# Kernel optimization log

Measured on AMD Instinct MI355X. Metric: run time of the kernel, lower is better.

The kernel has to match this reference:

```python
import jax, jax.numpy as jnp
import numpy as np

B, M = 16, 4096


def setup_inputs() -> dict:
    key = jax.random.key(0)
    k1, k2, k3, k4, k5 = jax.random.split(key, 5)
    return {
        "pred_R": jax.random.normal(k1, (B, 3, 3), dtype=jnp.float32),
        "pred_t": jax.random.normal(k2, (B, 3), dtype=jnp.float32),
        "gt_R": jax.random.normal(k3, (B, 3, 3), dtype=jnp.float32),
        "gt_t": jax.random.normal(k4, (B, 3), dtype=jnp.float32),
        "model_points": jax.random.normal(k5, (M, 3), dtype=jnp.float32),
    }


def reference(pred_R, pred_t, gt_R, gt_t, model_points):
    # Rigid transform: points @ R^T + t  -> [B, M, 3]
    pred = jnp.einsum('mk,bjk->bmj', model_points, pred_R) + pred_t[:, None, :]
    gt = jnp.einsum('mk,bjk->bmj', model_points, gt_R) + gt_t[:, None, :]
    # Pairwise squared L2 via ||a||^2 + ||b||^2 - 2 a.b (avoids [B,M,M,3] diff tensor)
    pn = jnp.sum(pred * pred, axis=-1)            # [B, M]
    gn = jnp.sum(gt * gt, axis=-1)                # [B, M]
    cross = jnp.einsum('bmk,bnk->bmn', pred, gt)  # [B, M, M]
    d2 = pn[:, :, None] + gn[:, None, :] - 2.0 * cross
    dist = jnp.sqrt(jnp.maximum(d2, 0.0))         # [B, M, M]
    min_dist = jnp.min(dist, axis=2)              # closest gt point per pred point
    return jnp.mean(min_dist)
```

## Files before the change

### kernel.cpp

```cpp
#include <hip/hip_runtime.h>
#include <hip/hip_bf16.h>
#include <float.h>

#define NB 16
#define MPTS 4096
#define NPRED (NB * MPTS)
#define GTQ 4
#define GTN 1024
#define NT 32
#define BLK 256
#define FRAGS 4
#define PREDS_PER_BLK 512
#define PGRP 8

typedef _Float16 half8 __attribute__((ext_vector_type(8)));
typedef float f32x16 __attribute__((ext_vector_type(16)));

__device__ inline void split16(float x, _Float16& hi, _Float16& lo) {
    hi = (_Float16)x;
    lo = (_Float16)(x - (float)hi);
}

__global__ __launch_bounds__(BLK) void adds_mfma(
    const float* __restrict__ pred_R, const float* __restrict__ pred_t,
    const float* __restrict__ gt_R,   const float* __restrict__ gt_t,
    const float* __restrict__ mp,     float* __restrict__ pmin,
    float* __restrict__ out)
{
    __shared__ half8 aT[NT * 64];

    const int bid = blockIdx.x;
    const int gtq = bid & (GTQ - 1);
    const int pg  = (bid >> 2) & (PGRP - 1);
    const int b   = bid >> 5;
    const int tid = threadIdx.x;
    const int ln  = tid & 63;
    const int wv  = tid >> 6;

    if (bid == 0 && tid == 0) out[0] = 0.0f;

    {
        float gR[9];
#pragma unroll
        for (int i = 0; i < 9; ++i) gR[i] = gt_R[b * 9 + i];
        const float gtx = gt_t[b * 3 + 0];
        const float gty = gt_t[b * 3 + 1];
        const float gtz = gt_t[b * 3 + 2];

#pragma unroll
        for (int w = 0; w < (NT * 64) / BLK; ++w) {
            const int v  = w * BLK + tid;
            const int t  = v >> 6;
            const int vl = v & 63;
            const int n  = gtq * GTN + t * 32 + (vl & 31);
            const float mx = mp[n * 3 + 0];
            const float my = mp[n * 3 + 1];
            const float mz = mp[n * 3 + 2];
            const float gx = fmaf(gR[0], mx, fmaf(gR[1], my, fmaf(gR[2], mz, gtx)));
            const float gy = fmaf(gR[3], mx, fmaf(gR[4], my, fmaf(gR[5], mz, gty)));
            const float gz = fmaf(gR[6], mx, fmaf(gR[7], my, fmaf(gR[8], mz, gtz)));
            const float gn = fmaf(gx, gx, fmaf(gy, gy, gz * gz));
            const float ux = -2.0f * gx, uy = -2.0f * gy, uz = -2.0f * gz;
            _Float16 hux, lux, huy, luy, huz, luz, gnh, gnl;
            split16(ux, hux, lux);
            split16(uy, huy, luy);
            split16(uz, huz, luz);
            split16(gn, gnh, gnl);
            half8 pk;
            if ((vl >> 5) == 0) {
                pk[0] = hux; pk[1] = huy; pk[2] = huz;
                pk[3] = hux; pk[4] = huy; pk[5] = huz;
                pk[6] = lux; pk[7] = luy;
            } else {
                pk[0] = luz; pk[1] = gnh; pk[2] = gnl;
                pk[3] = (_Float16)0.0f; pk[4] = (_Float16)0.0f;
                pk[5] = (_Float16)0.0f; pk[6] = (_Float16)0.0f;
                pk[7] = (_Float16)0.0f;
            }
            aT[v] = pk;
        }
    }

    float pR[9];
#pragma unroll
    for (int i = 0; i < 9; ++i) pR[i] = pred_R[b * 9 + i];
    const float ptx = pred_t[b * 3 + 0];
    const float pty = pred_t[b * 3 + 1];
    const float ptz = pred_t[b * 3 + 2];

    half8 bf[FRAGS];
    float pn[FRAGS];
    const int kh = ln >> 5;
#pragma unroll
    for (int f = 0; f < FRAGS; ++f) {
        const int predl = pg * PREDS_PER_BLK + wv * 128 + f * 32 + (ln & 31);
        const float mx = mp[predl * 3 + 0];
        const float my = mp[predl * 3 + 1];
        const float mz = mp[predl * 3 + 2];
        const float px = fmaf(pR[0], mx, fmaf(pR[1], my, fmaf(pR[2], mz, ptx)));
        const float py = fmaf(pR[3], mx, fmaf(pR[4], my, fmaf(pR[5], mz, pty)));
        const float pz = fmaf(pR[6], mx, fmaf(pR[7], my, fmaf(pR[8], mz, ptz)));
        pn[f] = fmaf(px, px, fmaf(py, py, pz * pz));
        _Float16 hpx, lpx, hpy, lpy, hpz, lpz;
        split16(px, hpx, lpx);
        split16(py, hpy, lpy);
        split16(pz, hpz, lpz);
        half8 v;
        if (kh == 0) {
            v[0] = hpx; v[1] = hpy; v[2] = hpz;
            v[3] = lpx; v[4] = lpy; v[5] = lpz;
            v[6] = hpx; v[7] = hpy;
        } else {
            v[0] = hpz; v[1] = (_Float16)1.0f; v[2] = (_Float16)1.0f;
            v[3] = (_Float16)0.0f; v[4] = (_Float16)0.0f;
            v[5] = (_Float16)0.0f; v[6] = (_Float16)0.0f;
            v[7] = (_Float16)0.0f;
        }
        bf[f] = v;
    }

    __syncthreads();

    f32x16 zc;
#pragma unroll
    for (int i = 0; i < 16; ++i) zc[i] = 0.0f;

    float best[FRAGS][8];
#pragma unroll
    for (int f = 0; f < FRAGS; ++f)
#pragma unroll
        for (int j = 0; j < 8; ++j) best[f][j] = FLT_MAX;

    half8 a_cur = aT[ln];
    for (int t = 0; t < NT; ++t) {
        const half8 a_nxt = (t + 1 < NT) ? aT[(t + 1) * 64 + ln] : a_cur;
        const f32x16 d0 = __builtin_amdgcn_mfma_f32_32x32x16_f16(a_cur, bf[0], zc, 0, 0, 0);
        const f32x16 d1 = __builtin_amdgcn_mfma_f32_32x32x16_f16(a_cur, bf[1], zc, 0, 0, 0);
        const f32x16 d2 = __builtin_amdgcn_mfma_f32_32x32x16_f16(a_cur, bf[2], zc, 0, 0, 0);
        const f32x16 d3 = __builtin_amdgcn_mfma_f32_32x32x16_f16(a_cur, bf[3], zc, 0, 0, 0);
#pragma unroll
        for (int j = 0; j < 8; ++j) {
            best[0][j] = fminf(best[0][j], fminf(d0[2 * j], d0[2 * j + 1]));
            best[1][j] = fminf(best[1][j], fminf(d1[2 * j], d1[2 * j + 1]));
            best[2][j] = fminf(best[2][j], fminf(d2[2 * j], d2[2 * j + 1]));
            best[3][j] = fminf(best[3][j], fminf(d3[2 * j], d3[2 * j + 1]));
        }
        a_cur = a_nxt;
    }

#pragma unroll
    for (int f = 0; f < FRAGS; ++f) {
        float r = fminf(fminf(fminf(best[f][0], best[f][1]), fminf(best[f][2], best[f][3])),
                        fminf(fminf(best[f][4], best[f][5]), fminf(best[f][6], best[f][7])));
        r = fminf(r, __shfl_xor(r, 32, 64));
        const float d2v = fmaxf(pn[f] + r, 0.0f);
        if (ln < 32) {
            const int predl = pg * PREDS_PER_BLK + wv * 128 + f * 32 + ln;
            pmin[gtq * NPRED + b * MPTS + predl] = d2v;
        }
    }
}

__global__ __launch_bounds__(1024) void adds_finish(
    const float* __restrict__ pmin, float* __restrict__ out)
{
    __shared__ float wsum[16];
    const int tid = threadIdx.x;
    const int g = blockIdx.x * 1024 + tid;
    const float m0 = fminf(pmin[0 * NPRED + g], pmin[1 * NPRED + g]);
    const float m1 = fminf(pmin[2 * NPRED + g], pmin[3 * NPRED + g]);
    float s = sqrtf(fminf(m0, m1));
#pragma unroll
    for (int off = 32; off > 0; off >>= 1) s += __shfl_down(s, off, 64);
    if ((tid & 63) == 0) wsum[tid >> 6] = s;
    __syncthreads();
    if (tid == 0) {
        float t = 0.0f;
#pragma unroll
        for (int w = 0; w < 16; ++w) t += wsum[w];
        atomicAdd(out, t * (1.0f / (float)NPRED));
    }
}

extern "C" void kernel_launch(void* const* d_in, const int* in_sizes, int n_in,
                              void* d_out, int out_size, void* d_ws, size_t ws_size,
                              hipStream_t stream) {
    const float* pred_R = (const float*)d_in[0];
    const float* pred_t = (const float*)d_in[1];
    const float* gt_R   = (const float*)d_in[2];
    const float* gt_t   = (const float*)d_in[3];
    const float* mp     = (const float*)d_in[4];
    float* out = (float*)d_out;
    float* pmin = (float*)d_ws;

    adds_mfma<<<dim3(NB * PGRP * GTQ), dim3(BLK), 0, stream>>>(
        pred_R, pred_t, gt_R, gt_t, mp, pmin, out);
    adds_finish<<<dim3(64), dim3(1024), 0, stream>>>(pmin, out);
}
```

Baseline: 22.38 us.

## Split gt points into eight chunks to double grid size and occupancy

```diff
diff --git a/kernel.cpp b/kernel.cpp
--- a/kernel.cpp
+++ b/kernel.cpp
@@ -5,9 +5,9 @@
 #define NB 16
 #define MPTS 4096
 #define NPRED (NB * MPTS)
-#define GTQ 4
-#define GTN 1024
-#define NT 32
+#define GTQ 8
+#define GTN 512
+#define NT 16
 #define BLK 256
 #define FRAGS 4
 #define PREDS_PER_BLK 512
@@ -21,7 +21,7 @@
     lo = (_Float16)(x - (float)hi);
 }
 
-__global__ __launch_bounds__(BLK) void adds_mfma(
+__global__ __launch_bounds__(BLK, 4) void adds_mfma(
     const float* __restrict__ pred_R, const float* __restrict__ pred_t,
     const float* __restrict__ gt_R,   const float* __restrict__ gt_t,
     const float* __restrict__ mp,     float* __restrict__ pmin,
@@ -31,8 +31,8 @@
 
     const int bid = blockIdx.x;
     const int gtq = bid & (GTQ - 1);
-    const int pg  = (bid >> 2) & (PGRP - 1);
-    const int b   = bid >> 5;
+    const int pg  = (bid >> 3) & (PGRP - 1);
+    const int b   = bid >> 6;
     const int tid = threadIdx.x;
     const int ln  = tid & 63;
     const int wv  = tid >> 6;
@@ -48,11 +48,9 @@
         const float gtz = gt_t[b * 3 + 2];
 
 #pragma unroll
-        for (int w = 0; w < (NT * 64) / BLK; ++w) {
-            const int v  = w * BLK + tid;
-            const int t  = v >> 6;
-            const int vl = v & 63;
-            const int n  = gtq * GTN + t * 32 + (vl & 31);
+        for (int j = 0; j < GTN / BLK; ++j) {
+            const int nl = j * BLK + tid;
+            const int n  = gtq * GTN + nl;
             const float mx = mp[n * 3 + 0];
             const float my = mp[n * 3 + 1];
             const float mz = mp[n * 3 + 2];
@@ -66,18 +64,16 @@
             split16(uy, huy, luy);
             split16(uz, huz, luz);
             split16(gn, gnh, gnl);
-            half8 pk;
-            if ((vl >> 5) == 0) {
-                pk[0] = hux; pk[1] = huy; pk[2] = huz;
-                pk[3] = hux; pk[4] = huy; pk[5] = huz;
-                pk[6] = lux; pk[7] = luy;
-            } else {
-                pk[0] = luz; pk[1] = gnh; pk[2] = gnl;
-                pk[3] = (_Float16)0.0f; pk[4] = (_Float16)0.0f;
-                pk[5] = (_Float16)0.0f; pk[6] = (_Float16)0.0f;
-                pk[7] = (_Float16)0.0f;
-            }
-            aT[v] = pk;
+            half8 k0, k1;
+            k0[0] = hux; k0[1] = huy; k0[2] = huz;
+            k0[3] = hux; k0[4] = huy; k0[5] = huz;
+            k0[6] = lux; k0[7] = luy;
+            k1[0] = luz; k1[1] = gnh; k1[2] = gnl;
+            k1[3] = (_Float16)0.0f; k1[4] = (_Float16)0.0f; k1[5] = (_Float16)0.0f;
+            k1[6] = (_Float16)0.0f; k1[7] = (_Float16)0.0f;
+            const int t = nl >> 5, r = nl & 31;
+            aT[t * 64 + r]      = k0;
+            aT[t * 64 + 32 + r] = k1;
         }
     }
 
@@ -134,16 +130,23 @@
     half8 a_cur = aT[ln];
     for (int t = 0; t < NT; ++t) {
         const half8 a_nxt = (t + 1 < NT) ? aT[(t + 1) * 64 + ln] : a_cur;
-        const f32x16 d0 = __builtin_amdgcn_mfma_f32_32x32x16_f16(a_cur, bf[0], zc, 0, 0, 0);
-        const f32x16 d1 = __builtin_amdgcn_mfma_f32_32x32x16_f16(a_cur, bf[1], zc, 0, 0, 0);
-        const f32x16 d2 = __builtin_amdgcn_mfma_f32_32x32x16_f16(a_cur, bf[2], zc, 0, 0, 0);
-        const f32x16 d3 = __builtin_amdgcn_mfma_f32_32x32x16_f16(a_cur, bf[3], zc, 0, 0, 0);
-#pragma unroll
-        for (int j = 0; j < 8; ++j) {
-            best[0][j] = fminf(best[0][j], fminf(d0[2 * j], d0[2 * j + 1]));
-            best[1][j] = fminf(best[1][j], fminf(d1[2 * j], d1[2 * j + 1]));
-            best[2][j] = fminf(best[2][j], fminf(d2[2 * j], d2[2 * j + 1]));
-            best[3][j] = fminf(best[3][j], fminf(d3[2 * j], d3[2 * j + 1]));
+        {
+            const f32x16 d0 = __builtin_amdgcn_mfma_f32_32x32x16_f16(a_cur, bf[0], zc, 0, 0, 0);
+            const f32x16 d1 = __builtin_amdgcn_mfma_f32_32x32x16_f16(a_cur, bf[1], zc, 0, 0, 0);
+#pragma unroll
+            for (int j = 0; j < 8; ++j) {
+                best[0][j] = fminf(best[0][j], fminf(d0[2 * j], d0[2 * j + 1]));
+                best[1][j] = fminf(best[1][j], fminf(d1[2 * j], d1[2 * j + 1]));
+            }
+        }
+        {
+            const f32x16 d2 = __builtin_amdgcn_mfma_f32_32x32x16_f16(a_cur, bf[2], zc, 0, 0, 0);
+            const f32x16 d3 = __builtin_amdgcn_mfma_f32_32x32x16_f16(a_cur, bf[3], zc, 0, 0, 0);
+#pragma unroll
+            for (int j = 0; j < 8; ++j) {
+                best[2][j] = fminf(best[2][j], fminf(d2[2 * j], d2[2 * j + 1]));
+                best[3][j] = fminf(best[3][j], fminf(d3[2 * j], d3[2 * j + 1]));
+            }
         }
         a_cur = a_nxt;
     }
@@ -161,14 +164,18 @@
     }
 }
 
-__global__ __launch_bounds__(1024) void adds_finish(
+__global__ __launch_bounds__(512) void adds_finish(
     const float* __restrict__ pmin, float* __restrict__ out)
 {
-    __shared__ float wsum[16];
+    __shared__ float wsum[8];
     const int tid = threadIdx.x;
-    const int g = blockIdx.x * 1024 + tid;
-    const float m0 = fminf(pmin[0 * NPRED + g], pmin[1 * NPRED + g]);
-    const float m1 = fminf(pmin[2 * NPRED + g], pmin[3 * NPRED + g]);
+    const int g = blockIdx.x * 512 + tid;
+    float m0 = FLT_MAX, m1 = FLT_MAX;
+#pragma unroll
+    for (int q = 0; q < GTQ; q += 2) {
+        m0 = fminf(m0, pmin[(q + 0) * NPRED + g]);
+        m1 = fminf(m1, pmin[(q + 1) * NPRED + g]);
+    }
     float s = sqrtf(fminf(m0, m1));
 #pragma unroll
     for (int off = 32; off > 0; off >>= 1) s += __shfl_down(s, off, 64);
@@ -177,7 +184,7 @@
     if (tid == 0) {
         float t = 0.0f;
 #pragma unroll
-        for (int w = 0; w < 16; ++w) t += wsum[w];
+        for (int w = 0; w < 8; ++w) t += wsum[w];
         atomicAdd(out, t * (1.0f / (float)NPRED));
     }
 }
@@ -195,5 +202,5 @@
 
     adds_mfma<<<dim3(NB * PGRP * GTQ), dim3(BLK), 0, stream>>>(
         pred_R, pred_t, gt_R, gt_t, mp, pmin, out);
-    adds_finish<<<dim3(64), dim3(1024), 0, stream>>>(pmin, out);
-}
+    adds_finish<<<dim3(NPRED / 512), dim3(512), 0, stream>>>(pmin, out);
+}
```

After: 19.17 us (median of 2 runs). 14.3% less time.
